# Optimization experiments

Hardware: AMD Instinct MI355X
Metric: run time of the kernel (lower is better)

The kernel has to match this reference:

```python
import jax, jax.numpy as jnp
import numpy as np

B, S, D, H = 2, 2048, 1024, 16
DK = D // H
EPS = 1e-5


def setup_inputs() -> dict:
    key = jax.random.key(0)
    ks = jax.random.split(key, 6)
    std = (2.0 / (D + D)) ** 0.5
    return {
        "x": jax.random.normal(ks[0], (B, S, D), dtype=jnp.float32),
        "W_Q": jax.random.normal(ks[1], (D, D), dtype=jnp.float32) * std,
        "W_K": jax.random.normal(ks[2], (D, D), dtype=jnp.float32) * std,
        "W_V": jax.random.normal(ks[3], (D, D), dtype=jnp.float32) * std,
        "W_O": jax.random.normal(ks[4], (D, D), dtype=jnp.float32) * std,
        "gain": jnp.ones((D,), dtype=jnp.float32),
        "positions": jnp.arange(S, dtype=jnp.int64 if jax.config.jax_enable_x64 else jnp.int32),
        "theta": 10000,
        "max_seq_len": 2048,
    }


def rmsnorm(x, gain):
    xf = x.astype(jnp.float32)
    rms = jnp.sqrt(jnp.mean(xf * xf, axis=-1, keepdims=True) + EPS)
    return ((xf / rms) * gain).astype(x.dtype)


def apply_rope(x, sin, cos):
    # x: [..., seq, dk]; sin/cos: [seq, dk//2] broadcast over leading dims
    x_even = x[..., 0::2]
    x_odd = x[..., 1::2]
    r_even = x_even * cos - x_odd * sin
    r_odd = x_odd * cos + x_even * sin
    return jnp.stack([r_even, r_odd], axis=-1).reshape(x.shape)


def reference(x, W_Q, W_K, W_V, W_O, gain, positions, theta, max_seq_len):
    seq_len = x.shape[-2]
    Q = jnp.einsum('od,bsd->bso', W_Q, x)
    K = jnp.einsum('od,bsd->bso', W_K, x)
    V = jnp.einsum('od,bsd->bso', W_V, x)
    # RMSNorm over full d_model BEFORE head split (as in original)
    Q = rmsnorm(Q, gain)
    K = rmsnorm(K, gain)
    # split heads: [b, h, s, dk]
    Q = Q.reshape(*Q.shape[:-1], H, DK).swapaxes(-3, -2)
    K = K.reshape(*K.shape[:-1], H, DK).swapaxes(-3, -2)
    V = V.reshape(*V.shape[:-1], H, DK).swapaxes(-3, -2)
    # RoPE tables
    exponents = 2.0 * jnp.arange(DK // 2, dtype=jnp.float32) / DK
    inv_freq = 1.0 / (jnp.float32(theta) ** exponents)
    angles = positions.astype(jnp.float32)[:, None] * inv_freq[None, :]  # [S, DK//2]
    sin, cos = jnp.sin(angles), jnp.cos(angles)
    Q = apply_rope(Q, sin, cos)
    K = apply_rope(K, sin, cos)
    # causal attention
    scores = jnp.einsum('bhqd,bhkd->bhqk', Q, K) / jnp.sqrt(jnp.float32(DK))
    causal = jnp.tril(jnp.ones((seq_len, seq_len), dtype=bool))
    scores = jnp.where(causal, scores, -jnp.inf)
    attn = jax.nn.softmax(scores, axis=-1)
    out = jnp.einsum('bhqk,bhkd->bhqd', attn, V)
    out = out.swapaxes(-3, -2).reshape(*x.shape[:-1], D)
    return jnp.einsum('of,bsf->bso', W_O, out)
```

## Files before the change

### kernel.cpp

```cpp
#include <hip/hip_runtime.h>
#include <hip/hip_bf16.h>

typedef __attribute__((ext_vector_type(8))) __bf16 bf16x8;
typedef __attribute__((ext_vector_type(4))) __bf16 bf16x4;
typedef __attribute__((ext_vector_type(4))) float  f32x4;
typedef __attribute__((ext_vector_type(4))) short  s16x4;

#define S_LEN 2048
#define D_DIM 1024
#define NH    16
#define GK    1024
#define GN    1024

__device__ __forceinline__ float fast_exp2(float x) {
#if __has_builtin(__builtin_amdgcn_exp2f)
  return __builtin_amdgcn_exp2f(x);
#else
  return exp2f(x);
#endif
}

__device__ __forceinline__ f32x4 mfma16(bf16x4 a, bf16x4 b, f32x4 c) {
#if __has_builtin(__builtin_amdgcn_mfma_f32_16x16x16_bf16)
  return __builtin_amdgcn_mfma_f32_16x16x16_bf16(a, b, c, 0, 0, 0);
#else
  return __builtin_amdgcn_mfma_f32_16x16x16bf16_1k(
      __builtin_bit_cast(s16x4, a), __builtin_bit_cast(s16x4, b), c, 0, 0, 0);
#endif
}

__device__ __forceinline__ void gld_lds16(const void* g, void* l) {
  __builtin_amdgcn_global_load_lds(
      (const __attribute__((address_space(1))) unsigned int*)g,
      (__attribute__((address_space(3))) unsigned int*)l, 16, 0, 0);
}

__global__ __launch_bounds__(256) void cast_all(
    const float* __restrict__ x,  const float* __restrict__ wq, const float* __restrict__ wk,
    const float* __restrict__ wv, const float* __restrict__ wo,
    __bf16* __restrict__ xb, __bf16* __restrict__ wqb, __bf16* __restrict__ wkb,
    __bf16* __restrict__ wvb, __bf16* __restrict__ wob)
{
  const int NTOT = 2 << 20;
  for (int i = blockIdx.x * 256 + threadIdx.x; i < NTOT; i += 1024 * 256) {
    const float* s; __bf16* d; int off;
    if (i < (1 << 20)) { s = x; d = xb; off = i; }
    else {
      const int j = i - (1 << 20);
      const int r = j >> 18; off = j & ((1 << 18) - 1);
      s = (r == 0) ? wq : (r == 1) ? wk : (r == 2) ? wv : wo;
      d = (r == 0) ? wqb : (r == 1) ? wkb : (r == 2) ? wvb : wob;
    }
    float4 v = ((const float4*)s)[off];
    bf16x4 o = { (__bf16)v.x, (__bf16)v.y, (__bf16)v.z, (__bf16)v.w };
    ((bf16x4*)d)[off] = o;
  }
}

__global__ __launch_bounds__(256, 6) void gemm_qkv(
    const __bf16* __restrict__ A,
    const __bf16* __restrict__ W0, const __bf16* __restrict__ W1, const __bf16* __restrict__ W2,
    __bf16* __restrict__ C0, __bf16* __restrict__ C1, __bf16* __restrict__ VtOut)
{
  const int bid = blockIdx.x;
  const int e = bid & 7, mg = e >> 1, ng = e & 1;
  const int q = bid >> 3;
  const int mode = q % 3;
  const int t = q / 3;
  const int m0 = (mg * 16 + (t & 15)) * 64;
  const int n0 = (ng * 4 + (t >> 4)) * 128;
  const __bf16* Wm = (mode == 0) ? W0 : (mode == 1) ? W1 : W2;

  __shared__ __align__(16) __bf16 As[64 * 64];
  __shared__ __align__(16) __bf16 Bs[128 * 64];

  const int tid  = threadIdx.x;
  const int lane = tid & 63;
  const int w    = tid >> 6;
  const int wr   = w >> 1, wc = w & 1;
  const int lm   = lane & 15, qd = lane >> 4;

  const __bf16* ap[2]; int loA[2];
  #pragma unroll
  for (int j = 0; j < 2; j++) {
    const int c = tid + 256 * j;
    const int r = c >> 3, cpos = c & 7;
    ap[j] = A + (size_t)(m0 + r) * GK + (cpos ^ (r & 7)) * 8;
    loA[j] = c * 8;
  }
  const __bf16* bp[4]; int loB[4];
  #pragma unroll
  for (int j = 0; j < 4; j++) {
    const int c = tid + 256 * j;
    const int r = c >> 3, cpos = c & 7;
    bp[j] = Wm + (size_t)(n0 + r) * GK + (cpos ^ (r & 7)) * 8;
    loB[j] = c * 8;
  }

  const int sw = lm & 7;

  f32x4 zero = {0.f, 0.f, 0.f, 0.f};
  f32x4 acc[2][4];
  #pragma unroll
  for (int i = 0; i < 2; i++)
    #pragma unroll
    for (int j = 0; j < 4; j++) acc[i][j] = zero;

  for (int k0 = 0; k0 < GK; k0 += 64) {
    #pragma unroll
    for (int j = 0; j < 2; j++) gld_lds16(ap[j] + k0, &As[loA[j]]);
    #pragma unroll
    for (int j = 0; j < 4; j++) gld_lds16(bp[j] + k0, &Bs[loB[j]]);
    __syncthreads();
    #pragma unroll
    for (int half = 0; half < 2; half++) {
      const int cph = ((qd + 4 * half) ^ sw) * 8;
      bf16x8 af[2], bfv[4];
      #pragma unroll
      for (int i = 0; i < 2; i++) af[i]  = *(const bf16x8*)&As[(wr * 32 + i * 16 + lm) * 64 + cph];
      #pragma unroll
      for (int j = 0; j < 4; j++) bfv[j] = *(const bf16x8*)&Bs[(wc * 64 + j * 16 + lm) * 64 + cph];
      #pragma unroll
      for (int i = 0; i < 2; i++)
        #pragma unroll
        for (int j = 0; j < 4; j++)
          acc[i][j] = __builtin_amdgcn_mfma_f32_16x16x32_bf16(af[i], bfv[j], acc[i][j], 0, 0, 0);
    }
    __syncthreads();
  }

  if (mode < 2) {
    __bf16* C = (mode == 0) ? C0 : C1;
    #pragma unroll
    for (int i = 0; i < 2; i++) {
      const int row = m0 + wr * 32 + i * 16 + qd * 4;
      #pragma unroll
      for (int j = 0; j < 4; j++) {
        const int col = n0 + wc * 64 + j * 16 + lm;
        #pragma unroll
        for (int r = 0; r < 4; r++)
          C[(size_t)(row + r) * GN + col] = (__bf16)acc[i][j][r];
      }
    }
  } else {
    #pragma unroll
    for (int i = 0; i < 2; i++) {
      const int row = m0 + wr * 32 + i * 16 + qd * 4;
      const int b = row >> 11, s = row & (S_LEN - 1);
      #pragma unroll
      for (int j = 0; j < 4; j++) {
        const int col = n0 + wc * 64 + j * 16 + lm;
        const int h = col >> 6, d = col & 63;
        bf16x4 o = { (__bf16)acc[i][j][0], (__bf16)acc[i][j][1],
                     (__bf16)acc[i][j][2], (__bf16)acc[i][j][3] };
        *(bf16x4*)(VtOut + (((size_t)(b * NH + h) * 64 + d) * S_LEN + s)) = o;
      }
    }
  }
}

__global__ __launch_bounds__(256, 6) void gemm_out64(
    const __bf16* __restrict__ A, const __bf16* __restrict__ Wm, float* __restrict__ C)
{
  const int bid = blockIdx.x;
  const int e = bid & 7, mg = e >> 1, ng = e & 1;
  const int q = bid >> 3;
  const int m0 = (mg * 16 + (q & 15)) * 64;
  const int n0 = (ng * 4 + (q >> 4)) * 128;

  __shared__ __align__(16) __bf16 As[64 * 64];
  __shared__ __align__(16) __bf16 Bs[128 * 64];

  const int tid  = threadIdx.x;
  const int lane = tid & 63;
  const int w    = tid >> 6;
  const int wr   = w >> 1, wc = w & 1;
  const int lm   = lane & 15, qd = lane >> 4;

  const __bf16* ap[2]; int loA[2];
  #pragma unroll
  for (int j = 0; j < 2; j++) {
    const int c = tid + 256 * j;
    const int r = c >> 3, cpos = c & 7;
    ap[j] = A + (size_t)(m0 + r) * GK + (cpos ^ (r & 7)) * 8;
    loA[j] = c * 8;
  }
  const __bf16* bp[4]; int loB[4];
  #pragma unroll
  for (int j = 0; j < 4; j++) {
    const int c = tid + 256 * j;
    const int r = c >> 3, cpos = c & 7;
    bp[j] = Wm + (size_t)(n0 + r) * GK + (cpos ^ (r & 7)) * 8;
    loB[j] = c * 8;
  }

  const int sw = lm & 7;

  f32x4 zero = {0.f, 0.f, 0.f, 0.f};
  f32x4 acc[2][4];
  #pragma unroll
  for (int i = 0; i < 2; i++)
    #pragma unroll
    for (int j = 0; j < 4; j++) acc[i][j] = zero;

  for (int k0 = 0; k0 < GK; k0 += 64) {
    #pragma unroll
    for (int j = 0; j < 2; j++) gld_lds16(ap[j] + k0, &As[loA[j]]);
    #pragma unroll
    for (int j = 0; j < 4; j++) gld_lds16(bp[j] + k0, &Bs[loB[j]]);
    __syncthreads();
    #pragma unroll
    for (int half = 0; half < 2; half++) {
      const int cph = ((qd + 4 * half) ^ sw) * 8;
      bf16x8 af[2], bfv[4];
      #pragma unroll
      for (int i = 0; i < 2; i++) af[i]  = *(const bf16x8*)&As[(wr * 32 + i * 16 + lm) * 64 + cph];
      #pragma unroll
      for (int j = 0; j < 4; j++) bfv[j] = *(const bf16x8*)&Bs[(wc * 64 + j * 16 + lm) * 64 + cph];
      #pragma unroll
      for (int i = 0; i < 2; i++)
        #pragma unroll
        for (int j = 0; j < 4; j++)
          acc[i][j] = __builtin_amdgcn_mfma_f32_16x16x32_bf16(af[i], bfv[j], acc[i][j], 0, 0, 0);
    }
    __syncthreads();
  }

  #pragma unroll
  for (int i = 0; i < 2; i++) {
    const int row = m0 + wr * 32 + i * 16 + qd * 4;
    #pragma unroll
    for (int j = 0; j < 4; j++) {
      const int col = n0 + wc * 64 + j * 16 + lm;
      #pragma unroll
      for (int r = 0; r < 4; r++)
        C[(size_t)(row + r) * GN + col] = acc[i][j][r];
    }
  }
}

__global__ __launch_bounds__(256) void norm_rope(
    const __bf16* __restrict__ Qf, const __bf16* __restrict__ Kf,
    const float* __restrict__ gain, const int* __restrict__ positions,
    const int* __restrict__ theta_p,
    __bf16* __restrict__ Qh, __bf16* __restrict__ Kh)
{
  const int row = blockIdx.x;
  const int s = row & (S_LEN - 1), b = row >> 11;
  const int t = threadIdx.x, d0 = t * 4;

  const bf16x4 qv = *(const bf16x4*)(Qf + (size_t)row * D_DIM + d0);
  const bf16x4 kv = *(const bf16x4*)(Kf + (size_t)row * D_DIM + d0);
  const float q0 = (float)qv[0], q1 = (float)qv[1], q2 = (float)qv[2], q3 = (float)qv[3];
  const float k0 = (float)kv[0], k1 = (float)kv[1], k2 = (float)kv[2], k3 = (float)kv[3];

  float sq = q0 * q0 + q1 * q1 + q2 * q2 + q3 * q3;
  float sk = k0 * k0 + k1 * k1 + k2 * k2 + k3 * k3;
  #pragma unroll
  for (int off = 32; off; off >>= 1) { sq += __shfl_xor(sq, off); sk += __shfl_xor(sk, off); }
  __shared__ float red[8];
  const int lane = t & 63, wv = t >> 6;
  if (lane == 0) { red[wv] = sq; red[4 + wv] = sk; }
  __syncthreads();
  sq = red[0] + red[1] + red[2] + red[3];
  sk = red[4] + red[5] + red[6] + red[7];
  const float SC2 = 0.125f * 1.44269504089f;
  const float invq = rsqrtf(sq * (1.0f / 1024.0f) + 1e-5f) * SC2;
  const float invk = rsqrtf(sk * (1.0f / 1024.0f) + 1e-5f);

  const float4 g = *(const float4*)(gain + d0);
  const float qn0 = q0 * invq * g.x, qn1 = q1 * invq * g.y;
  const float qn2 = q2 * invq * g.z, qn3 = q3 * invq * g.w;
  const float kn0 = k0 * invk * g.x, kn1 = k1 * invk * g.y;
  const float kn2 = k2 * invk * g.z, kn3 = k3 * invk * g.w;

  const float pos = (float)positions[s];
  const float th  = (float)theta_p[0];
  const int idx = d0 & 63, h = d0 >> 6, p0 = idx >> 1;
  const float lg32 = __log2f(th) * (1.0f / 32.0f);
  const float f0 = fast_exp2(-(float)p0 * lg32);
  const float f1 = fast_exp2(-(float)(p0 + 1) * lg32);
  float s0, cc0, s1, cc1;
  __sincosf(pos * f0, &s0, &cc0);
  __sincosf(pos * f1, &s1, &cc1);

  const float qe0 = qn0 * cc0 - qn1 * s0, qo0 = qn1 * cc0 + qn0 * s0;
  const float qe1 = qn2 * cc1 - qn3 * s1, qo1 = qn3 * cc1 + qn2 * s1;
  const float ke0 = kn0 * cc0 - kn1 * s0, ko0 = kn1 * cc0 + kn0 * s0;
  const float ke1 = kn2 * cc1 - kn3 * s1, ko1 = kn3 * cc1 + kn2 * s1;

  const size_t obase = ((size_t)((b * NH + h) * S_LEN + s)) * 64 + idx;
  bf16x4 qo = { (__bf16)qe0, (__bf16)qo0, (__bf16)qe1, (__bf16)qo1 };
  bf16x4 ko = { (__bf16)ke0, (__bf16)ko0, (__bf16)ke1, (__bf16)ko1 };
  *(bf16x4*)(Qh + obase) = qo;
  *(bf16x4*)(Kh + obase) = ko;
}

__global__ __launch_bounds__(256) void attn_fwd(
    const __bf16* __restrict__ Qh, const __bf16* __restrict__ Kh,
    const __bf16* __restrict__ Vt, __bf16* __restrict__ Ob)
{
  const int bid = blockIdx.x;
  const int g   = bid >> 5, gj = g & 7, gs = g >> 3;
  const int qt  = (gs == 0) ? 31 - gj : (gs == 1) ? gj : (gs == 2) ? 23 - gj : 8 + gj;
  const int rr  = bid & 31;
  const int bh  = (rr & 7) * 4 + (rr >> 3);
  const int tid = threadIdx.x, lane = tid & 63, w = tid >> 6;
  const int lm = lane & 15, qd = lane >> 4;

  __shared__ __align__(16) __bf16 smem[8192 + 8192];
  __bf16* Ks = smem;
  __bf16* Vs = smem + 8192;

  const int row0 = qt * 64 + w * 16;
  const int qglob = row0 + lm;
  const size_t qbase = (size_t)bh * S_LEN * 64;
  const bf16x8 aq0 = *(const bf16x8*)(Qh + qbase + (size_t)qglob * 64 + qd * 8);
  const bf16x8 aq1 = *(const bf16x8*)(Qh + qbase + (size_t)qglob * 64 + 32 + qd * 8);

  const __bf16* Kb = Kh + (size_t)bh * S_LEN * 64;
  const __bf16* Vb = Vt + (size_t)bh * 64 * S_LEN;
  const int c0 = tid, c1 = 256 + tid;
  const int kr0 = c0 >> 3, kr1 = c1 >> 3;
  const int kg0 = ((c0 & 7) ^ (kr0 & 7)) * 8;
  const int kg1 = ((c1 & 7) ^ (kr1 & 7)) * 8;
  const int cpA = (qd ^ (lm & 7)) * 8;
  const int cpB = cpA ^ 32;

  auto stage = [&](int buf, int k0) {
    __bf16* Kd = Ks + buf * 4096;
    __bf16* Vd = Vs + buf * 4096;
    gld_lds16(Kb + (size_t)(k0 + kr0) * 64 + kg0, &Kd[c0 * 8]);
    gld_lds16(Kb + (size_t)(k0 + kr1) * 64 + kg1, &Kd[c1 * 8]);
    gld_lds16(Vb + (size_t)kr0 * S_LEN + k0 + kg0, &Vd[c0 * 8]);
    gld_lds16(Vb + (size_t)kr1 * S_LEN + k0 + kg1, &Vd[c1 * 8]);
  };

  f32x4 zero = {0.f, 0.f, 0.f, 0.f};
  f32x4 lacc = zero;
  f32x4 o[4];
  #pragma unroll
  for (int jb = 0; jb < 4; jb++) o[jb] = zero;

  bf16x4 ones4;
  #pragma unroll
  for (int i = 0; i < 4; i++) ones4[i] = (__bf16)1.0f;

  stage(0, 0);

  for (int kt = 0; kt <= qt; ++kt) {
    const int cur = kt & 1;
    __syncthreads();
    if (kt < qt) stage(cur ^ 1, (kt + 1) * 64);

    const __bf16* Kc = Ks + cur * 4096;
    const __bf16* Vc = Vs + cur * 4096;
    const int k0 = kt * 64;
    const bool diag = (kt == qt);

    bf16x4 pfrag[4];
    #pragma unroll
    for (int kb = 0; kb < 4; kb++) {
      const int krow = (kb * 16 + lm) * 64;
      const bf16x8 ak0 = *(const bf16x8*)&Kc[krow + cpA];
      const bf16x8 ak1 = *(const bf16x8*)&Kc[krow + cpB];
      f32x4 sc = zero;
      sc = __builtin_amdgcn_mfma_f32_16x16x32_bf16(ak0, aq0, sc, 0, 0, 0);
      sc = __builtin_amdgcn_mfma_f32_16x16x32_bf16(ak1, aq1, sc, 0, 0, 0);
      float p[4];
      if (diag) {
        const int keyb = k0 + kb * 16 + qd * 4;
        #pragma unroll
        for (int r = 0; r < 4; r++)
          p[r] = (keyb + r <= qglob) ? fast_exp2(sc[r]) : 0.f;
      } else {
        #pragma unroll
        for (int r = 0; r < 4; r++) p[r] = fast_exp2(sc[r]);
      }
      bf16x4 pf = { (__bf16)p[0], (__bf16)p[1], (__bf16)p[2], (__bf16)p[3] };
      pfrag[kb] = pf;
      lacc = mfma16(ones4, pf, lacc);
    }

    #pragma unroll
    for (int jb = 0; jb < 4; jb++) {
      const int vrow = jb * 16 + lm;
      const int rsw = vrow & 7;
      #pragma unroll
      for (int kb = 0; kb < 4; kb++) {
        const int c = 2 * kb + (qd >> 1);
        const bf16x4 av = *(const bf16x4*)&Vc[vrow * 64 + ((c ^ rsw) << 3) + (qd & 1) * 4];
        o[jb] = mfma16(av, pfrag[kb], o[jb]);
      }
    }
  }

  const int b = bh >> 4, h = bh & 15;
  const float inv = 1.0f / lacc[0];
  const size_t base = ((size_t)(b * S_LEN + qglob)) * D_DIM + h * 64 + qd * 4;
  #pragma unroll
  for (int jb = 0; jb < 4; jb++) {
    bf16x4 ov = { (__bf16)(o[jb][0] * inv), (__bf16)(o[jb][1] * inv),
                  (__bf16)(o[jb][2] * inv), (__bf16)(o[jb][3] * inv) };
    *(bf16x4*)(Ob + base + jb * 16) = ov;
  }
}

extern "C" void kernel_launch(void* const* d_in, const int* in_sizes, int n_in,
                              void* d_out, int out_size, void* d_ws, size_t ws_size,
                              hipStream_t stream)
{
  (void)in_sizes; (void)n_in; (void)out_size; (void)ws_size;
  const float* x    = (const float*)d_in[0];
  const float* WQ   = (const float*)d_in[1];
  const float* WK   = (const float*)d_in[2];
  const float* WV   = (const float*)d_in[3];
  const float* WO   = (const float*)d_in[4];
  const float* gain = (const float*)d_in[5];
  const int* positions = (const int*)d_in[6];
  const int* theta     = (const int*)d_in[7];
  float* out = (float*)d_out;

  char* ws = (char*)d_ws;
  const size_t MB = 1024 * 1024;
  __bf16* xb  = (__bf16*)(ws + 0);
  __bf16* WQb = (__bf16*)(ws + 8  * MB);
  __bf16* WKb = (__bf16*)(ws + 10 * MB);
  __bf16* WVb = (__bf16*)(ws + 12 * MB);
  __bf16* WOb = (__bf16*)(ws + 14 * MB);
  __bf16* Qfb = (__bf16*)(ws + 16 * MB);
  __bf16* Kfb = (__bf16*)(ws + 24 * MB);
  __bf16* Vt  = (__bf16*)(ws + 32 * MB);
  __bf16* Qh  = (__bf16*)(ws + 40 * MB);
  __bf16* Kh  = (__bf16*)(ws + 48 * MB);
  __bf16* Ob  = (__bf16*)(ws + 56 * MB);

  cast_all<<<1024, 256, 0, stream>>>(x, WQ, WK, WV, WO, xb, WQb, WKb, WVb, WOb);
  gemm_qkv<<<1536, 256, 0, stream>>>(xb, WQb, WKb, WVb, Qfb, Kfb, Vt);
  norm_rope<<<4096, 256, 0, stream>>>(Qfb, Kfb, gain, positions, theta, Qh, Kh);
  attn_fwd<<<1024, 256, 0, stream>>>(Qh, Kh, Vt, Ob);
  gemm_out64<<<512, 256, 0, stream>>>(Ob, WOb, out);
}
```

Baseline: 175.1 us.

## Double-buffer LDS in projection GEMMs with 32-wide K tiles

```diff
diff --git a/kernel.cpp b/kernel.cpp
--- a/kernel.cpp
+++ b/kernel.cpp
@@ -71,8 +71,8 @@
   const int n0 = (ng * 4 + (t >> 4)) * 128;
   const __bf16* Wm = (mode == 0) ? W0 : (mode == 1) ? W1 : W2;
 
-  __shared__ __align__(16) __bf16 As[64 * 64];
-  __shared__ __align__(16) __bf16 Bs[128 * 64];
+  __shared__ __align__(16) __bf16 As[2][64 * 32];
+  __shared__ __align__(16) __bf16 Bs[2][128 * 32];
 
   const int tid  = threadIdx.x;
   const int lane = tid & 63;
@@ -80,24 +80,25 @@
   const int wr   = w >> 1, wc = w & 1;
   const int lm   = lane & 15, qd = lane >> 4;
 
-  const __bf16* ap[2]; int loA[2];
+  const int ca = tid, ra = ca >> 2, cpa = ca & 3;
+  const __bf16* ap = A + (size_t)(m0 + ra) * GK + (cpa ^ (ra & 3) ^ ((ra >> 2) & 1)) * 8;
+  const int loA = ca * 8;
+  const __bf16* bp[2]; int loB[2];
   #pragma unroll
   for (int j = 0; j < 2; j++) {
     const int c = tid + 256 * j;
-    const int r = c >> 3, cpos = c & 7;
-    ap[j] = A + (size_t)(m0 + r) * GK + (cpos ^ (r & 7)) * 8;
-    loA[j] = c * 8;
-  }
-  const __bf16* bp[4]; int loB[4];
-  #pragma unroll
-  for (int j = 0; j < 4; j++) {
-    const int c = tid + 256 * j;
-    const int r = c >> 3, cpos = c & 7;
-    bp[j] = Wm + (size_t)(n0 + r) * GK + (cpos ^ (r & 7)) * 8;
+    const int rb = c >> 2, cpb = c & 3;
+    bp[j] = Wm + (size_t)(n0 + rb) * GK + (cpb ^ (rb & 3) ^ ((rb >> 2) & 1)) * 8;
     loB[j] = c * 8;
   }
 
-  const int sw = lm & 7;
+  const int cp = (qd ^ (lm & 3) ^ ((lm >> 2) & 1)) * 8;
+
+  auto stage = [&](int buf, int k0) {
+    gld_lds16(ap + k0,    &As[buf][loA]);
+    gld_lds16(bp[0] + k0, &Bs[buf][loB[0]]);
+    gld_lds16(bp[1] + k0, &Bs[buf][loB[1]]);
+  };
 
   f32x4 zero = {0.f, 0.f, 0.f, 0.f};
   f32x4 acc[2][4];
@@ -106,27 +107,21 @@
     #pragma unroll
     for (int j = 0; j < 4; j++) acc[i][j] = zero;
 
-  for (int k0 = 0; k0 < GK; k0 += 64) {
-    #pragma unroll
-    for (int j = 0; j < 2; j++) gld_lds16(ap[j] + k0, &As[loA[j]]);
-    #pragma unroll
-    for (int j = 0; j < 4; j++) gld_lds16(bp[j] + k0, &Bs[loB[j]]);
+  stage(0, 0);
+  for (int k0 = 0; k0 < GK; k0 += 32) {
+    const int cur = (k0 >> 5) & 1;
     __syncthreads();
-    #pragma unroll
-    for (int half = 0; half < 2; half++) {
-      const int cph = ((qd + 4 * half) ^ sw) * 8;
-      bf16x8 af[2], bfv[4];
-      #pragma unroll
-      for (int i = 0; i < 2; i++) af[i]  = *(const bf16x8*)&As[(wr * 32 + i * 16 + lm) * 64 + cph];
-      #pragma unroll
-      for (int j = 0; j < 4; j++) bfv[j] = *(const bf16x8*)&Bs[(wc * 64 + j * 16 + lm) * 64 + cph];
-      #pragma unroll
-      for (int i = 0; i < 2; i++)
-        #pragma unroll
-        for (int j = 0; j < 4; j++)
-          acc[i][j] = __builtin_amdgcn_mfma_f32_16x16x32_bf16(af[i], bfv[j], acc[i][j], 0, 0, 0);
-    }
-    __syncthreads();
+    if (k0 + 32 < GK) stage(cur ^ 1, k0 + 32);
+    bf16x8 af[2], bfv[4];
+    #pragma unroll
+    for (int i = 0; i < 2; i++) af[i]  = *(const bf16x8*)&As[cur][(wr * 32 + i * 16 + lm) * 32 + cp];
+    #pragma unroll
+    for (int j = 0; j < 4; j++) bfv[j] = *(const bf16x8*)&Bs[cur][(wc * 64 + j * 16 + lm) * 32 + cp];
+    #pragma unroll
+    for (int i = 0; i < 2; i++)
+      #pragma unroll
+      for (int j = 0; j < 4; j++)
+        acc[i][j] = __builtin_amdgcn_mfma_f32_16x16x32_bf16(af[i], bfv[j], acc[i][j], 0, 0, 0);
   }
 
   if (mode < 2) {
@@ -168,8 +163,8 @@
   const int m0 = (mg * 16 + (q & 15)) * 64;
   const int n0 = (ng * 4 + (q >> 4)) * 128;
 
-  __shared__ __align__(16) __bf16 As[64 * 64];
-  __shared__ __align__(16) __bf16 Bs[128 * 64];
+  __shared__ __align__(16) __bf16 As[2][64 * 32];
+  __shared__ __align__(16) __bf16 Bs[2][128 * 32];
 
   const int tid  = threadIdx.x;
   const int lane = tid & 63;
@@ -177,24 +172,25 @@
   const int wr   = w >> 1, wc = w & 1;
   const int lm   = lane & 15, qd = lane >> 4;
 
-  const __bf16* ap[2]; int loA[2];
+  const int ca = tid, ra = ca >> 2, cpa = ca & 3;
+  const __bf16* ap = A + (size_t)(m0 + ra) * GK + (cpa ^ (ra & 3) ^ ((ra >> 2) & 1)) * 8;
+  const int loA = ca * 8;
+  const __bf16* bp[2]; int loB[2];
   #pragma unroll
   for (int j = 0; j < 2; j++) {
     const int c = tid + 256 * j;
-    const int r = c >> 3, cpos = c & 7;
-    ap[j] = A + (size_t)(m0 + r) * GK + (cpos ^ (r & 7)) * 8;
-    loA[j] = c * 8;
-  }
-  const __bf16* bp[4]; int loB[4];
-  #pragma unroll
-  for (int j = 0; j < 4; j++) {
-    const int c = tid + 256 * j;
-    const int r = c >> 3, cpos = c & 7;
-    bp[j] = Wm + (size_t)(n0 + r) * GK + (cpos ^ (r & 7)) * 8;
+    const int rb = c >> 2, cpb = c & 3;
+    bp[j] = Wm + (size_t)(n0 + rb) * GK + (cpb ^ (rb & 3) ^ ((rb >> 2) & 1)) * 8;
     loB[j] = c * 8;
   }
 
-  const int sw = lm & 7;
+  const int cp = (qd ^ (lm & 3) ^ ((lm >> 2) & 1)) * 8;
+
+  auto stage = [&](int buf, int k0) {
+    gld_lds16(ap + k0,    &As[buf][loA]);
+    gld_lds16(bp[0] + k0, &Bs[buf][loB[0]]);
+    gld_lds16(bp[1] + k0, &Bs[buf][loB[1]]);
+  };
 
   f32x4 zero = {0.f, 0.f, 0.f, 0.f};
   f32x4 acc[2][4];
@@ -203,27 +199,21 @@
     #pragma unroll
     for (int j = 0; j < 4; j++) acc[i][j] = zero;
 
-  for (int k0 = 0; k0 < GK; k0 += 64) {
-    #pragma unroll
-    for (int j = 0; j < 2; j++) gld_lds16(ap[j] + k0, &As[loA[j]]);
-    #pragma unroll
-    for (int j = 0; j < 4; j++) gld_lds16(bp[j] + k0, &Bs[loB[j]]);
+  stage(0, 0);
+  for (int k0 = 0; k0 < GK; k0 += 32) {
+    const int cur = (k0 >> 5) & 1;
     __syncthreads();
-    #pragma unroll
-    for (int half = 0; half < 2; half++) {
-      const int cph = ((qd + 4 * half) ^ sw) * 8;
-      bf16x8 af[2], bfv[4];
-      #pragma unroll
-      for (int i = 0; i < 2; i++) af[i]  = *(const bf16x8*)&As[(wr * 32 + i * 16 + lm) * 64 + cph];
-      #pragma unroll
-      for (int j = 0; j < 4; j++) bfv[j] = *(const bf16x8*)&Bs[(wc * 64 + j * 16 + lm) * 64 + cph];
-      #pragma unroll
-      for (int i = 0; i < 2; i++)
-        #pragma unroll
-        for (int j = 0; j < 4; j++)
-          acc[i][j] = __builtin_amdgcn_mfma_f32_16x16x32_bf16(af[i], bfv[j], acc[i][j], 0, 0, 0);
-    }
-    __syncthreads();
+    if (k0 + 32 < GK) stage(cur ^ 1, k0 + 32);
+    bf16x8 af[2], bfv[4];
+    #pragma unroll
+    for (int i = 0; i < 2; i++) af[i]  = *(const bf16x8*)&As[cur][(wr * 32 + i * 16 + lm) * 32 + cp];
+    #pragma unroll
+    for (int j = 0; j < 4; j++) bfv[j] = *(const bf16x8*)&Bs[cur][(wc * 64 + j * 16 + lm) * 32 + cp];
+    #pragma unroll
+    for (int i = 0; i < 2; i++)
+      #pragma unroll
+      for (int j = 0; j < 4; j++)
+        acc[i][j] = __builtin_amdgcn_mfma_f32_16x16x32_bf16(af[i], bfv[j], acc[i][j], 0, 0, 0);
   }
 
   #pragma unroll
```

Result: slower. 195.3 us (+11.5%).
